# Performance work log

Hardware: AMD Instinct MI355X
Metric: run time of the kernel (lower is better)

The kernel has to match this reference:

```python
import jax, jax.numpy as jnp
import numpy as np
from jax import lax

B, L, D, E, K, H = 8, 1024, 256, 8, 2, 1024  # batch, seq(in_channel), in_dim, experts, top_k, out_channel/hidden
LMAX = L // 2  # largest expert input dim (factor i+2 = 2)
LENS = [L // (i + 2) for i in range(E)]


def setup_inputs() -> dict:
    key = jax.random.key(0)
    ks = jax.random.split(key, 12)
    x = jax.random.normal(ks[0], (B, L, D), dtype=jnp.float32)
    conv_ws = jax.random.normal(ks[1], (3, D, D, 3), dtype=jnp.float32) / np.sqrt(3 * D)
    conv_bs = jax.random.normal(ks[2], (3, D), dtype=jnp.float32) * 0.01
    fl_w = jax.random.normal(ks[3], (E, L), dtype=jnp.float32) / np.sqrt(L)
    fl_b = jax.random.normal(ks[4], (E,), dtype=jnp.float32) * 0.01
    # expert first-layer weights, zero-padded on input axis to LMAX (expert i uses L//(i+2) inputs)
    w1 = jax.random.normal(ks[5], (E, H, LMAX), dtype=jnp.float32) / np.sqrt(LMAX)
    col_mask = (np.arange(LMAX)[None, :] < np.array(LENS)[:, None]).astype(np.float32)  # [E, LMAX]
    w1 = w1 * jnp.asarray(col_mask)[:, None, :]
    b1 = jax.random.normal(ks[6], (E, H), dtype=jnp.float32) * 0.01
    w2 = jax.random.normal(ks[7], (E, H, H), dtype=jnp.float32) / np.sqrt(H)
    b2 = jax.random.normal(ks[8], (E, H), dtype=jnp.float32) * 0.01
    w3 = jax.random.normal(ks[9], (E, H, H), dtype=jnp.float32) / np.sqrt(H)
    b3 = jax.random.normal(ks[10], (E, H), dtype=jnp.float32) * 0.01
    return {"x": x, "conv_ws": conv_ws, "conv_bs": conv_bs, "fl_w": fl_w, "fl_b": fl_b,
            "w1": w1, "b1": b1, "w2": w2, "b2": b2, "w3": w3, "b3": b3}


def _gelu(v):
    return jax.nn.gelu(v, approximate=False)  # torch nn.GELU default is exact erf


def _forward(x, conv_ws, conv_bs, fl_w, fl_b, w1, b1, w2, b2, w3, b3):
    xt = jnp.transpose(x, (0, 2, 1))  # [B, D, L]
    # --- Router: 3 dilated causal-padded ('same') convs + GELU ---
    h = xt
    for i in range(3):
        d = 2 ** i
        h = lax.conv_general_dilated(h, conv_ws[i], window_strides=(1,), padding=[(d, d)],
                                     rhs_dilation=(d,), dimension_numbers=("NCH", "OIH", "NCH"))
        h = _gelu(h + conv_bs[i][None, :, None])
    logits = jax.nn.sigmoid(jnp.einsum("bdl,el->bde", h, fl_w) + fl_b)  # [B, D, E]
    prob = jax.nn.softmax(logits, axis=-1)
    top_val, top_idx = lax.top_k(prob, K)  # [B, D, K]
    top_val = top_val / jnp.sum(top_val, axis=-1, keepdims=True)
    # combine gate per expert: gates[b,d,e] = sum_k top_val * 1[top_idx==e]
    gates = jnp.sum(top_val[..., None] * jax.nn.one_hot(top_idx, E, dtype=top_val.dtype), axis=2)  # [B, D, E]
    # --- Per-expert downsample (avg_pool1d, kernel=stride=i+2), zero-padded to LMAX ---
    xs = []
    for i in range(E):
        f = i + 2
        Li = LENS[i]
        xd = xt[:, :, :Li * f].reshape(B, D, Li, f).mean(-1)  # [B, D, Li]
        xs.append(jnp.pad(xd, ((0, 0), (0, 0), (0, LMAX - Li))))
    xe = jnp.stack(xs)  # [E, B, D, LMAX]; pad cols align with zeroed w1 cols
    # --- Expert MLPs (dense compute, masked by gates; zero gate == token not routed) ---
    h1 = _gelu(jnp.einsum("ebdl,ehl->ebdh", xe, w1) + b1[:, None, None, :])
    h2 = _gelu(jnp.einsum("ebdh,egh->ebdg", h1, w2) + b2[:, None, None, :])
    h3 = jnp.einsum("ebdg,eog->ebdo", h2, w3) + b3[:, None, None, :]  # [E, B, D, H]
    out = jnp.einsum("ebdo,bde->bdo", h3, gates)  # scatter-add combine, [B, D, H]
    return jnp.transpose(out, (0, 2, 1))  # [B, L(out_channel), D]


def reference(x, conv_ws, conv_bs, fl_w, fl_b, w1, b1, w2, b2, w3, b3):
    return _forward(x, conv_ws, conv_bs, fl_w, fl_b, w1, b1, w2, b2, w3, b3)
```

## Files before the change

kernel.cpp:

```cpp
#include <hip/hip_runtime.h>
#include <math.h>

#define Bb 8
#define Ll 1024
#define Dd 256
#define Ee 8
#define Hh 1024
#define LMAXc 512
#define NTOK (Bb*Dd)
#define LPAD 1032
#define MAXTILES 72

typedef short bf16x8 __attribute__((ext_vector_type(8)));
typedef float f32x4 __attribute__((ext_vector_type(4)));
typedef unsigned short u16x8 __attribute__((ext_vector_type(8)));

__device__ __forceinline__ float gelu_f(float x) {
    return 0.5f * x * (1.0f + erff(x * 0.70710678118654752440f));
}
__device__ __forceinline__ unsigned short f2b(float x) {
    unsigned int u = __float_as_uint(x);
    return (unsigned short)((u + 0x7fffu + ((u >> 16) & 1u)) >> 16);
}
__device__ __forceinline__ float b2f(unsigned short h) {
    return __uint_as_float(((unsigned int)h) << 16);
}
__device__ __forceinline__ void gl_lds16(const void* g, void* l) {
    __builtin_amdgcn_global_load_lds((const __attribute__((address_space(1))) unsigned int*)g,
                                     (__attribute__((address_space(3))) unsigned int*)l, 16, 0, 0);
}
__device__ __forceinline__ void split_store(float4 v,
                                            unsigned short* __restrict__ hi,
                                            unsigned short* __restrict__ lo, int idx) {
    ushort2 h01, h23, l01, l23;
    unsigned short h;
    h = f2b(v.x); h01.x = h; l01.x = f2b(v.x - b2f(h));
    h = f2b(v.y); h01.y = h; l01.y = f2b(v.y - b2f(h));
    h = f2b(v.z); h23.x = h; l23.x = f2b(v.z - b2f(h));
    h = f2b(v.w); h23.y = h; l23.y = f2b(v.w - b2f(h));
    ((ushort2*)hi)[idx * 2] = h01; ((ushort2*)hi)[idx * 2 + 1] = h23;
    ((ushort2*)lo)[idx * 2] = l01; ((ushort2*)lo)[idx * 2 + 1] = l23;
}
__device__ __forceinline__ void cvt_store(float4 v, unsigned short* __restrict__ dst, int idx) {
    ushort2 h01, h23;
    h01.x = f2b(v.x); h01.y = f2b(v.y);
    h23.x = f2b(v.z); h23.y = f2b(v.w);
    ((ushort2*)dst)[idx * 2] = h01; ((ushort2*)dst)[idx * 2 + 1] = h23;
}

__global__ __launch_bounds__(256) void prep_all(
    const float* __restrict__ x, const float* __restrict__ cw,
    const float* __restrict__ w1, const float* __restrict__ w2,
    const float* __restrict__ w3,
    unsigned short* __restrict__ xhi, unsigned short* __restrict__ xlo,
    unsigned short* __restrict__ chi, unsigned short* __restrict__ clo,
    unsigned short* __restrict__ wchi, unsigned short* __restrict__ wclo,
    unsigned short* __restrict__ w1hi, unsigned short* __restrict__ w1lo,
    unsigned short* __restrict__ w2b, unsigned short* __restrict__ w3b,
    unsigned short* __restrict__ xe)
{
    int blk = blockIdx.x;
    int t = threadIdx.x;
    if (blk < 4096) {
        int u = blk;
        int e = u >> 9;
        int b = (u >> 6) & 7;
        int c = u & 63;
        int f = e + 2;
        int Li = Ll / f;
        int j0 = c * 8;
        if (j0 >= Li) return;
        int d = t;
        float invf = 1.0f / (float)f;
        int lim = Li - 1;
        float v[8] = {};
        for (int r = 0; r < f; ++r) {
            #pragma unroll
            for (int jj = 0; jj < 8; ++jj) {
                int j = j0 + jj; if (j > lim) j = lim;
                v[jj] += x[((size_t)(b * Ll + j * f + r)) * Dd + d];
            }
        }
        size_t obase = ((size_t)(e * NTOK + b * 256 + d)) * LMAXc + j0;
        if (j0 + 8 <= Li) {
            u16x8 hv;
            #pragma unroll
            for (int q = 0; q < 8; ++q) hv[q] = (short)f2b(v[q] * invf);
            *(u16x8*)(xe + obase) = hv;
        } else {
            for (int jj = 0; jj < Li - j0; ++jj)
                xe[obase + jj] = f2b(v[jj] * invf);
        }
    } else if (blk < 4128) {
        int u = (blk - 4096) * 256 + t;
        int f = u >> 11;
        int rem = u & 2047;
        int b = rem >> 8;
        int r2 = rem & 255;
        int row = r2 >> 5;
        int col = (r2 & 31) * 8;
        int padrow = (row < 4) ? row : (1024 + row);
        unsigned short* buf = (f == 0) ? xhi : (f == 1) ? xlo : (f == 2) ? chi : clo;
        u16x8 z = {0, 0, 0, 0, 0, 0, 0, 0};
        *(u16x8*)(buf + (size_t)(b * LPAD + padrow) * Dd + col) = z;
    } else if (blk < 4640) {
        int base = (blk - 4128) * 1024 + t;
        float4 v[4];
        #pragma unroll
        for (int it = 0; it < 4; ++it) v[it] = ((const float4*)x)[base + it * 256];
        #pragma unroll
        for (int it = 0; it < 4; ++it) {
            int idx = base + it * 256;
            int d4 = idx & 63;
            int l  = (idx >> 6) & 1023;
            int b  = idx >> 16;
            size_t o = ((size_t)(b * LPAD + 4 + l) * Dd + d4 * 4) >> 1;
            ushort2 h01, h23, l01, l23;
            unsigned short h;
            h = f2b(v[it].x); h01.x = h; l01.x = f2b(v[it].x - b2f(h));
            h = f2b(v[it].y); h01.y = h; l01.y = f2b(v[it].y - b2f(h));
            h = f2b(v[it].z); h23.x = h; l23.x = f2b(v[it].z - b2f(h));
            h = f2b(v[it].w); h23.y = h; l23.y = f2b(v[it].w - b2f(h));
            ((ushort2*)xhi)[o] = h01; ((ushort2*)xhi)[o + 1] = h23;
            ((ushort2*)xlo)[o] = l01; ((ushort2*)xlo)[o + 1] = l23;
        }
    } else if (blk < 5216) {
        int base = (blk - 4640) * 1024 + t;
        float vv[4];
        #pragma unroll
        for (int it = 0; it < 4; ++it) {
            int idx = base + it * 256;
            int i = idx & (Dd - 1);
            int o = (idx >> 8) & (Dd - 1);
            int lk = idx >> 16;
            int layer = lk / 3;
            int k = lk % 3;
            vv[it] = cw[(((size_t)layer * Dd + o) * Dd + i) * 3 + k];
        }
        #pragma unroll
        for (int it = 0; it < 4; ++it) {
            int idx = base + it * 256;
            unsigned short h = f2b(vv[it]);
            wchi[idx] = h;
            wclo[idx] = f2b(vv[it] - b2f(h));
        }
    } else if (blk < 6240) {
        int base = (blk - 5216) * 1024 + t;
        float4 v[4];
        #pragma unroll
        for (int it = 0; it < 4; ++it) v[it] = ((const float4*)w1)[base + it * 256];
        #pragma unroll
        for (int it = 0; it < 4; ++it) split_store(v[it], w1hi, w1lo, base + it * 256);
    } else if (blk < 8288) {
        int base = (blk - 6240) * 1024 + t;
        float4 v[4];
        #pragma unroll
        for (int it = 0; it < 4; ++it) v[it] = ((const float4*)w2)[base + it * 256];
        #pragma unroll
        for (int it = 0; it < 4; ++it) cvt_store(v[it], w2b, base + it * 256);
    } else {
        int base = (blk - 8288) * 1024 + t;
        float4 v[4];
        #pragma unroll
        for (int it = 0; it < 4; ++it) v[it] = ((const float4*)w3)[base + it * 256];
        #pragma unroll
        for (int it = 0; it < 4; ++it) cvt_store(v[it], w3b, base + it * 256);
    }
}

template<int MODE>
__global__ __launch_bounds__(256, 2) void conv_mfma(
    const unsigned short* __restrict__ inhi, const unsigned short* __restrict__ inlo,
    const unsigned short* __restrict__ whiL, const unsigned short* __restrict__ wloL,
    const float* __restrict__ bias,
    unsigned short* __restrict__ outhi, unsigned short* __restrict__ outlo,
    const float* __restrict__ flw, float* __restrict__ logits, int dil)
{
    __shared__ char smem[32768];
    char* sAhi = smem;
    char* sAlo = smem + 8192;
    char* sBhi = smem + 16384;
    char* sBlo = smem + 24576;

    const int t = threadIdx.x;
    const int lane = t & 63, w = t >> 6;
    const int r16 = lane & 15, quad = lane >> 4;
    const int wr = w >> 1, wc = w & 1;
    const int row0 = blockIdx.x * 64;
    const int col0 = blockIdx.y * 64;
    const int b = row0 >> 10, l0 = row0 & 1023;

    int aoff[2], boff[2];
    #pragma unroll
    for (int i = 0; i < 2; ++i) {
        int ra = wr * 32 + i * 16 + r16;
        aoff[i] = ra * 64 + ((quad ^ ((ra >> 1) & 3)) << 4);
        int rb = wc * 32 + i * 16 + r16;
        boff[i] = rb * 64 + ((quad ^ ((rb >> 1) & 3)) << 4);
    }
    const int rs = t >> 2, ce = ((t & 3) ^ ((rs >> 1) & 3)) << 3;
    const unsigned short* gAhi = inhi + (size_t)(b * LPAD + 4 + l0 + rs) * Dd + ce;
    const unsigned short* gAlo = inlo + (size_t)(b * LPAD + 4 + l0 + rs) * Dd + ce;

    f32x4 acc[2][2];
    const f32x4 zero4 = {0.f, 0.f, 0.f, 0.f};
    #pragma unroll
    for (int i = 0; i < 2; ++i)
        #pragma unroll
        for (int j = 0; j < 2; ++j) acc[i][j] = zero4;

    for (int tap = 0; tap < 3; ++tap) {
        const int sh = (tap - 1) * dil;
        const unsigned short* pAhi = gAhi + sh * Dd;
        const unsigned short* pAlo = gAlo + sh * Dd;
        const unsigned short* gBhi = whiL + ((size_t)tap * Dd + col0 + rs) * Dd + ce;
        const unsigned short* gBlo = wloL + ((size_t)tap * Dd + col0 + rs) * Dd + ce;
        for (int kb = 0; kb < Dd; kb += 64) {
            gl_lds16(pAhi + kb,      sAhi + (w << 10));
            gl_lds16(pAhi + kb + 32, sAhi + 4096 + (w << 10));
            gl_lds16(pAlo + kb,      sAlo + (w << 10));
            gl_lds16(pAlo + kb + 32, sAlo + 4096 + (w << 10));
            gl_lds16(gBhi + kb,      sBhi + (w << 10));
            gl_lds16(gBhi + kb + 32, sBhi + 4096 + (w << 10));
            gl_lds16(gBlo + kb,      sBlo + (w << 10));
            gl_lds16(gBlo + kb + 32, sBlo + 4096 + (w << 10));
            __syncthreads();
            #pragma unroll
            for (int h = 0; h < 2; ++h) {
                const int ho = h * 4096;
                bf16x8 ah[2], al[2], bh[2], bl[2];
                #pragma unroll
                for (int i = 0; i < 2; ++i) {
                    ah[i] = *(const bf16x8*)(sAhi + ho + aoff[i]);
                    al[i] = *(const bf16x8*)(sAlo + ho + aoff[i]);
                    bh[i] = *(const bf16x8*)(sBhi + ho + boff[i]);
                    bl[i] = *(const bf16x8*)(sBlo + ho + boff[i]);
                }
                #pragma unroll
                for (int mi = 0; mi < 2; ++mi)
                    #pragma unroll
                    for (int ni = 0; ni < 2; ++ni) {
                        acc[mi][ni] = __builtin_amdgcn_mfma_f32_16x16x32_bf16(ah[mi], bh[ni], acc[mi][ni], 0, 0, 0);
                        acc[mi][ni] = __builtin_amdgcn_mfma_f32_16x16x32_bf16(ah[mi], bl[ni], acc[mi][ni], 0, 0, 0);
                        acc[mi][ni] = __builtin_amdgcn_mfma_f32_16x16x32_bf16(al[mi], bh[ni], acc[mi][ni], 0, 0, 0);
                    }
            }
            __syncthreads();
        }
    }

    int cc[2]; float bv[2];
    #pragma unroll
    for (int ni = 0; ni < 2; ++ni) {
        cc[ni] = col0 + wc * 32 + ni * 16 + r16;
        bv[ni] = bias[cc[ni]];
    }
    if (MODE == 0) {
        #pragma unroll
        for (int mi = 0; mi < 2; ++mi) {
            int lb = l0 + wr * 32 + mi * 16 + quad * 4;
            #pragma unroll
            for (int reg = 0; reg < 4; ++reg) {
                int l = lb + reg;
                #pragma unroll
                for (int ni = 0; ni < 2; ++ni) {
                    float v = gelu_f(acc[mi][ni][reg] + bv[ni]);
                    size_t o = (size_t)(b * LPAD + 4 + l) * Dd + cc[ni];
                    unsigned short h = f2b(v);
                    outhi[o] = h;
                    outlo[o] = f2b(v - b2f(h));
                }
            }
        }
    } else {
        float* wl   = (float*)smem;
        float* slog = (float*)(smem + 2048);
        for (int i = t; i < 512; i += 256) {
            int ll = i >> 3, e = i & 7;
            wl[i] = flw[e * Ll + l0 + ll];
            slog[i] = 0.0f;
        }
        __syncthreads();
        float part[2][8];
        #pragma unroll
        for (int ni = 0; ni < 2; ++ni)
            #pragma unroll
            for (int e = 0; e < 8; ++e) part[ni][e] = 0.0f;
        #pragma unroll
        for (int mi = 0; mi < 2; ++mi) {
            #pragma unroll
            for (int reg = 0; reg < 4; ++reg) {
                int ll = wr * 32 + mi * 16 + quad * 4 + reg;
                #pragma unroll
                for (int ni = 0; ni < 2; ++ni) {
                    float v = gelu_f(acc[mi][ni][reg] + bv[ni]);
                    #pragma unroll
                    for (int e = 0; e < 8; ++e) part[ni][e] += v * wl[ll * 8 + e];
                }
            }
        }
        #pragma unroll
        for (int ni = 0; ni < 2; ++ni) {
            int dl = wc * 32 + ni * 16 + r16;
            #pragma unroll
            for (int e = 0; e < 8; ++e) atomicAdd(&slog[dl * 8 + e], part[ni][e]);
        }
        __syncthreads();
        for (int i = t; i < 512; i += 256) {
            int dl = i >> 3, e = i & 7;
            atomicAdd(&logits[(size_t)(b * Dd + col0 + dl) * Ee + e], slog[i]);
        }
    }
}

template<int MODE, int GATHER, int TWOPASS>
__global__ __launch_bounds__(256, 4) void gemm_sp(
    const unsigned short* __restrict__ AG,
    const unsigned short* __restrict__ BhiG, const unsigned short* __restrict__ BloG,
    const float* __restrict__ biasG, const float* __restrict__ gates,
    const int* __restrict__ cntG, const int* __restrict__ listG,
    const int* __restrict__ tileTab, const int* __restrict__ ntiles,
    unsigned short* __restrict__ Cout, float* __restrict__ outf,
    int M, int N, int K)
{
    if (blockIdx.y >= ntiles[0]) return;
    const int desc = tileTab[blockIdx.y];
    const int e = desc >> 16;
    const int row0 = (desc & 0xffff) * 64;
    const int cn = cntG[e];

    constexpr int NCH = TWOPASS ? 2 : 4;
    __shared__ char smem[TWOPASS ? 24576 : 32768];
    char* sA   = smem;
    char* sBhi = smem + NCH * 4096;
    char* sBlo = smem + 2 * NCH * 4096;

    const unsigned short* Bhi = BhiG + (size_t)e * N * K;
    const unsigned short* Blo = TWOPASS ? (BloG + (size_t)e * N * K) : nullptr;
    const float* bias = biasG + (size_t)e * N;

    int Keff = K;
    if (GATHER) {
        int Li = Ll / (e + 2);
        Keff = ((Li + 63) >> 6) << 6;
    }

    const int t = threadIdx.x;
    const int lane = t & 63, w = t >> 6;
    const int r16 = lane & 15, quad = lane >> 4;
    const int wr = w >> 1, wc = w & 1;
    const int col0 = blockIdx.x * 64;

    int aoff[2], boff[2];
    #pragma unroll
    for (int i = 0; i < 2; ++i) {
        int ra = wr * 32 + i * 16 + r16;
        aoff[i] = ra * 64 + ((quad ^ ((ra >> 1) & 3)) << 4);
        int rb = wc * 32 + i * 16 + r16;
        boff[i] = rb * 64 + ((quad ^ ((rb >> 1) & 3)) << 4);
    }
    const int r0s = t >> 2, c0s = ((t & 3) ^ ((r0s >> 1) & 3)) << 3;
    int ri = row0 + r0s; if (ri > cn - 1) ri = cn - 1;
    const int ar = GATHER ? listG[e * NTOK + ri] : ri;
    const unsigned short* gA  = AG + ((size_t)e * M + ar) * K + c0s;
    const unsigned short* gB  = Bhi + (size_t)(col0 + r0s) * K + c0s;
    const unsigned short* gBl = TWOPASS ? (Blo + (size_t)(col0 + r0s) * K + c0s) : nullptr;
    const int wofs = w << 10;

    f32x4 acc[2][2];
    const f32x4 zero4 = {0.f, 0.f, 0.f, 0.f};
    #pragma unroll
    for (int i = 0; i < 2; ++i)
        #pragma unroll
        for (int j = 0; j < 2; ++j) acc[i][j] = zero4;

    for (int k0 = 0; k0 < Keff; k0 += NCH * 32) {
        #pragma unroll
        for (int c = 0; c < NCH; ++c) {
            gl_lds16(gA + k0 + c * 32, sA + c * 4096 + wofs);
            gl_lds16(gB + k0 + c * 32, sBhi + c * 4096 + wofs);
        }
        if (TWOPASS) {
            #pragma unroll
            for (int c = 0; c < NCH; ++c)
                gl_lds16(gBl + k0 + c * 32, sBlo + c * 4096 + wofs);
        }
        __syncthreads();
        #pragma unroll
        for (int h = 0; h < NCH; ++h) {
            const int ho = h * 4096;
            bf16x8 ah[2], bh[2];
            #pragma unroll
            for (int i = 0; i < 2; ++i) {
                ah[i] = *(const bf16x8*)(sA + ho + aoff[i]);
                bh[i] = *(const bf16x8*)(sBhi + ho + boff[i]);
            }
            #pragma unroll
            for (int mi = 0; mi < 2; ++mi)
                #pragma unroll
                for (int ni = 0; ni < 2; ++ni)
                    acc[mi][ni] = __builtin_amdgcn_mfma_f32_16x16x32_bf16(ah[mi], bh[ni], acc[mi][ni], 0, 0, 0);
            if (TWOPASS) {
                bf16x8 bl[2];
                #pragma unroll
                for (int i = 0; i < 2; ++i) bl[i] = *(const bf16x8*)(sBlo + ho + boff[i]);
                #pragma unroll
                for (int mi = 0; mi < 2; ++mi)
                    #pragma unroll
                    for (int ni = 0; ni < 2; ++ni)
                        acc[mi][ni] = __builtin_amdgcn_mfma_f32_16x16x32_bf16(ah[mi], bl[ni], acc[mi][ni], 0, 0, 0);
            }
        }
        __syncthreads();
    }

    int cc[2]; float bv[2];
    #pragma unroll
    for (int ni = 0; ni < 2; ++ni) {
        cc[ni] = col0 + wc * 32 + ni * 16 + r16;
        bv[ni] = bias[cc[ni]];
    }
    if (MODE == 0) {
        unsigned short* CE = Cout + (size_t)e * M * N;
        #pragma unroll
        for (int mi = 0; mi < 2; ++mi) {
            int rb = row0 + wr * 32 + mi * 16 + quad * 4;
            #pragma unroll
            for (int reg = 0; reg < 4; ++reg) {
                size_t roff = (size_t)(rb + reg) * N;
                #pragma unroll
                for (int ni = 0; ni < 2; ++ni)
                    CE[roff + cc[ni]] = f2b(gelu_f(acc[mi][ni][reg] + bv[ni]));
            }
        }
    } else {
        #pragma unroll
        for (int mi = 0; mi < 2; ++mi) {
            int rb = row0 + wr * 32 + mi * 16 + quad * 4;
            #pragma unroll
            for (int reg = 0; reg < 4; ++reg) {
                int i = rb + reg;
                if (i < cn) {
                    int tok = listG[e * NTOK + i];
                    float g = gates[(size_t)tok * Ee + e];
                    size_t roff = (size_t)tok * N;
                    #pragma unroll
                    for (int ni = 0; ni < 2; ++ni)
                        atomicAdd(&outf[roff + cc[ni]], g * (acc[mi][ni][reg] + bv[ni]));
                }
            }
        }
    }
}


__global__ __launch_bounds__(1024) void gates_final(const float* __restrict__ logits,
                                                    const float* __restrict__ fl_b,
                                                    float* __restrict__ gates,
                                                    int* __restrict__ cnt,
                                                    int* __restrict__ list,
                                                    int* __restrict__ tileTab,
                                                    int* __restrict__ ntiles) {
    __shared__ int scnt[Ee];
    if (threadIdx.x < Ee) scnt[threadIdx.x] = 0;
    __syncthreads();
    const int lane = threadIdx.x & 63;
    const unsigned long long ltmask = (1ull << lane) - 1ull;

    for (int tok = threadIdx.x; tok < NTOK; tok += 1024) {
        float s[Ee];
        #pragma unroll
        for (int e = 0; e < Ee; ++e) {
            float z = logits[tok * Ee + e] + fl_b[e];
            s[e] = 1.0f / (1.0f + expf(-z));
        }
        float mx = s[0];
        #pragma unroll
        for (int e = 1; e < Ee; ++e) mx = fmaxf(mx, s[e]);
        float p[Ee];
        #pragma unroll
        for (int e = 0; e < Ee; ++e) p[e] = expf(s[e] - mx);
        int i1 = 0;
        #pragma unroll
        for (int e = 1; e < Ee; ++e) if (p[e] > p[i1]) i1 = e;
        int i2 = (i1 == 0) ? 1 : 0;
        #pragma unroll
        for (int e = 0; e < Ee; ++e) {
            if (e == i1 || e == i2) continue;
            if (p[e] > p[i2]) i2 = e;
        }
        float inv = 1.0f / (p[i1] + p[i2]);
        #pragma unroll
        for (int e = 0; e < Ee; ++e) gates[tok * Ee + e] = 0.0f;
        gates[tok * Ee + i1] = p[i1] * inv;
        gates[tok * Ee + i2] = p[i2] * inv;

        #pragma unroll
        for (int slot = 0; slot < 2; ++slot) {
            int ie = slot ? i2 : i1;
            for (int e = 0; e < Ee; ++e) {
                unsigned long long m = __ballot(ie == e);
                if (m) {
                    int leader = __ffsll((long long)m) - 1;
                    int base = 0;
                    if (lane == leader) base = atomicAdd(&scnt[e], (int)__popcll(m));
                    base = __shfl(base, leader);
                    if (ie == e) {
                        int pos = base + (int)__popcll(m & ltmask);
                        list[e * NTOK + pos] = tok;
                    }
                }
            }
        }
    }
    __syncthreads();
    if (threadIdx.x < Ee) cnt[threadIdx.x] = scnt[threadIdx.x];
    if (threadIdx.x == 0) {
        int nt = 0;
        for (int e = 0; e < Ee; ++e) {
            int c = scnt[e];
            for (int m = 0; m * 64 < c; ++m) tileTab[nt++] = (e << 16) | m;
        }
        ntiles[0] = nt;
    }
}

__global__ __launch_bounds__(256) void transpose_out(const float* __restrict__ outacc,
                                                     float* __restrict__ out) {
    __shared__ float tile[32][33];
    int b = blockIdx.z;
    int d0 = blockIdx.x * 32;
    int o0 = blockIdx.y * 32;
    int tx = threadIdx.x & 31, ty = threadIdx.x >> 5;
    for (int i = 0; i < 32; i += 8)
        tile[ty + i][tx] = outacc[((size_t)b * Dd + d0 + ty + i) * Hh + o0 + tx];
    __syncthreads();
    for (int i = 0; i < 32; i += 8)
        out[((size_t)b * Hh + o0 + ty + i) * Dd + d0 + tx] = tile[tx][ty + i];
}

extern "C" void kernel_launch(void* const* d_in, const int* in_sizes, int n_in,
                              void* d_out, int out_size, void* d_ws, size_t ws_size,
                              hipStream_t stream) {
    const float* x       = (const float*)d_in[0];
    const float* conv_w  = (const float*)d_in[1];
    const float* conv_b  = (const float*)d_in[2];
    const float* fl_w    = (const float*)d_in[3];
    const float* fl_b    = (const float*)d_in[4];
    const float* w1      = (const float*)d_in[5];
    const float* b1      = (const float*)d_in[6];
    const float* w2      = (const float*)d_in[7];
    const float* b2      = (const float*)d_in[8];
    const float* w3      = (const float*)d_in[9];
    const float* b3      = (const float*)d_in[10];
    float* out = (float*)d_out;

    char* ws = (char*)d_ws;
    unsigned short* xphi = (unsigned short*)(ws);
    unsigned short* xplo = (unsigned short*)(ws + 4227072);
    unsigned short* cphi = (unsigned short*)(ws + 8454144);
    unsigned short* cplo = (unsigned short*)(ws + 12681216);
    unsigned short* wchi = (unsigned short*)(ws + 16908288);
    unsigned short* wclo = (unsigned short*)(ws + 18087936);
    unsigned short* h1   = (unsigned short*)(ws);
    unsigned short* h2   = (unsigned short*)(ws + 33554432);
    unsigned short* xe   = (unsigned short*)(ws + 67108864);
    unsigned short* w1hi = (unsigned short*)(ws + 83886080);
    unsigned short* w1lo = (unsigned short*)(ws + 92274688);
    unsigned short* w2b  = (unsigned short*)(ws + 100663296);
    unsigned short* w3b  = (unsigned short*)(ws + 117440512);
    float* logits  = (float*)(ws + 134217728);
    int*   cnt     = (int*)(ws + 134283264);
    int*   ntiles  = (int*)(ws + 134283296);
    int*   tileTab = (int*)(ws + 134283328);
    float* gates   = (float*)(ws + 134284288);
    int*   list    = (int*)(ws + 134349824);
    float* outacc  = (float*)(ws);

    hipMemsetAsync(logits, 0, 65536 + 64, stream);

    prep_all<<<10336, 256, 0, stream>>>(x, conv_w, w1, w2, w3,
                                        xphi, xplo, cphi, cplo, wchi, wclo,
                                        w1hi, w1lo, w2b, w3b, xe);

    const int WL = 3 * Dd * Dd;
    conv_mfma<0><<<dim3(Bb * Ll / 64, Dd / 64), 256, 0, stream>>>(
        xphi, xplo, wchi + 0 * WL, wclo + 0 * WL, conv_b + 0 * Dd, cphi, cplo, nullptr, nullptr, 1);
    conv_mfma<0><<<dim3(Bb * Ll / 64, Dd / 64), 256, 0, stream>>>(
        cphi, cplo, wchi + 1 * WL, wclo + 1 * WL, conv_b + 1 * Dd, xphi, xplo, nullptr, nullptr, 2);
    conv_mfma<1><<<dim3(Bb * Ll / 64, Dd / 64), 256, 0, stream>>>(
        xphi, xplo, wchi + 2 * WL, wclo + 2 * WL, conv_b + 2 * Dd, nullptr, nullptr, fl_w, logits, 4);

    gates_final<<<1, 1024, 0, stream>>>(logits, fl_b, gates, cnt, list, tileTab, ntiles);

    gemm_sp<0, 1, 1><<<dim3(16, MAXTILES), 256, 0, stream>>>(
        xe, w1hi, w1lo, b1, nullptr, cnt, list, tileTab, ntiles, h1, nullptr, NTOK, Hh, LMAXc);

    gemm_sp<0, 0, 0><<<dim3(16, MAXTILES), 256, 0, stream>>>(
        h1, w2b, nullptr, b2, nullptr, cnt, list, tileTab, ntiles, h2, nullptr, NTOK, Hh, Hh);

    hipMemsetAsync(outacc, 0, (size_t)NTOK * Hh * sizeof(float), stream);

    gemm_sp<1, 0, 0><<<dim3(16, MAXTILES), 256, 0, stream>>>(
        h2, w3b, nullptr, b3, gates, cnt, list, tileTab, ntiles, nullptr, outacc, NTOK, Hh, Hh);

    transpose_out<<<dim3(Dd / 32, Hh / 32, Bb), 256, 0, stream>>>(outacc, out);
}
```

Measured before the change: 308.2 us.

## Overlap expert weight bf16 conversion with conv kernels via extra grid blocks

Moves the w1/w2/w3 fp32-to-bf16 conversion out of the prep kernel and into extra blockIdx.y rows of the three conv kernels, so the memory-bound conversion runs alongside the compute-bound conv MFMA blocks. It also widens the x and conv-weight split conversions to 8-element vector stores. The conv kernels gain a template flag and more blocks, which may perturb scheduling, but the prep launch shrinks.

New measurement: 309.5 us. No clear change (+0.4%).

```diff
diff --git a/kernel.cpp b/kernel.cpp
--- a/kernel.cpp
+++ b/kernel.cpp
@@ -29,34 +29,12 @@
     __builtin_amdgcn_global_load_lds((const __attribute__((address_space(1))) unsigned int*)g,
                                      (__attribute__((address_space(3))) unsigned int*)l, 16, 0, 0);
 }
-__device__ __forceinline__ void split_store(float4 v,
-                                            unsigned short* __restrict__ hi,
-                                            unsigned short* __restrict__ lo, int idx) {
-    ushort2 h01, h23, l01, l23;
-    unsigned short h;
-    h = f2b(v.x); h01.x = h; l01.x = f2b(v.x - b2f(h));
-    h = f2b(v.y); h01.y = h; l01.y = f2b(v.y - b2f(h));
-    h = f2b(v.z); h23.x = h; l23.x = f2b(v.z - b2f(h));
-    h = f2b(v.w); h23.y = h; l23.y = f2b(v.w - b2f(h));
-    ((ushort2*)hi)[idx * 2] = h01; ((ushort2*)hi)[idx * 2 + 1] = h23;
-    ((ushort2*)lo)[idx * 2] = l01; ((ushort2*)lo)[idx * 2 + 1] = l23;
-}
-__device__ __forceinline__ void cvt_store(float4 v, unsigned short* __restrict__ dst, int idx) {
-    ushort2 h01, h23;
-    h01.x = f2b(v.x); h01.y = f2b(v.y);
-    h23.x = f2b(v.z); h23.y = f2b(v.w);
-    ((ushort2*)dst)[idx * 2] = h01; ((ushort2*)dst)[idx * 2 + 1] = h23;
-}
 
 __global__ __launch_bounds__(256) void prep_all(
     const float* __restrict__ x, const float* __restrict__ cw,
-    const float* __restrict__ w1, const float* __restrict__ w2,
-    const float* __restrict__ w3,
     unsigned short* __restrict__ xhi, unsigned short* __restrict__ xlo,
     unsigned short* __restrict__ chi, unsigned short* __restrict__ clo,
     unsigned short* __restrict__ wchi, unsigned short* __restrict__ wclo,
-    unsigned short* __restrict__ w1hi, unsigned short* __restrict__ w1lo,
-    unsigned short* __restrict__ w2b, unsigned short* __restrict__ w3b,
     unsigned short* __restrict__ xe)
 {
     int blk = blockIdx.x;
@@ -103,80 +81,100 @@
         unsigned short* buf = (f == 0) ? xhi : (f == 1) ? xlo : (f == 2) ? chi : clo;
         u16x8 z = {0, 0, 0, 0, 0, 0, 0, 0};
         *(u16x8*)(buf + (size_t)(b * LPAD + padrow) * Dd + col) = z;
-    } else if (blk < 4640) {
-        int base = (blk - 4128) * 1024 + t;
-        float4 v[4];
-        #pragma unroll
-        for (int it = 0; it < 4; ++it) v[it] = ((const float4*)x)[base + it * 256];
+    } else if (blk < 4384) {
+        int cb = blk - 4128;
+        const float4* s4 = (const float4*)x;
+        size_t ob = (size_t)cb * 1024 + t;
+        float4 v[8];
         #pragma unroll
         for (int it = 0; it < 4; ++it) {
-            int idx = base + it * 256;
-            int d4 = idx & 63;
-            int l  = (idx >> 6) & 1023;
-            int b  = idx >> 16;
-            size_t o = ((size_t)(b * LPAD + 4 + l) * Dd + d4 * 4) >> 1;
-            ushort2 h01, h23, l01, l23;
-            unsigned short h;
-            h = f2b(v[it].x); h01.x = h; l01.x = f2b(v[it].x - b2f(h));
-            h = f2b(v[it].y); h01.y = h; l01.y = f2b(v[it].y - b2f(h));
-            h = f2b(v[it].z); h23.x = h; l23.x = f2b(v[it].z - b2f(h));
-            h = f2b(v[it].w); h23.y = h; l23.y = f2b(v[it].w - b2f(h));
-            ((ushort2*)xhi)[o] = h01; ((ushort2*)xhi)[o + 1] = h23;
-            ((ushort2*)xlo)[o] = l01; ((ushort2*)xlo)[o + 1] = l23;
-        }
-    } else if (blk < 5216) {
-        int base = (blk - 4640) * 1024 + t;
-        float vv[4];
+            v[2 * it]     = s4[(ob + it * 256) * 2];
+            v[2 * it + 1] = s4[(ob + it * 256) * 2 + 1];
+        }
         #pragma unroll
         for (int it = 0; it < 4; ++it) {
-            int idx = base + it * 256;
+            size_t o = ob + it * 256;
+            int d8 = (int)(o & 31), l = (int)((o >> 5) & 1023), b = (int)(o >> 15);
+            size_t ooff = (size_t)(b * LPAD + 4 + l) * Dd + d8 * 8;
+            float vv[8] = {v[2*it].x, v[2*it].y, v[2*it].z, v[2*it].w,
+                           v[2*it+1].x, v[2*it+1].y, v[2*it+1].z, v[2*it+1].w};
+            u16x8 hv, lv;
+            #pragma unroll
+            for (int q = 0; q < 8; ++q) {
+                unsigned short h = f2b(vv[q]);
+                hv[q] = (short)h;
+                lv[q] = (short)f2b(vv[q] - b2f(h));
+            }
+            *(u16x8*)(xhi + ooff) = hv;
+            *(u16x8*)(xlo + ooff) = lv;
+        }
+    } else {
+        int cb = blk - 4384;
+        int idx0 = (cb * 256 + t) * 8;
+        float vv[8];
+        #pragma unroll
+        for (int q = 0; q < 8; ++q) {
+            int idx = idx0 + q;
             int i = idx & (Dd - 1);
             int o = (idx >> 8) & (Dd - 1);
             int lk = idx >> 16;
             int layer = lk / 3;
             int k = lk % 3;
-            vv[it] = cw[(((size_t)layer * Dd + o) * Dd + i) * 3 + k];
-        }
-        #pragma unroll
-        for (int it = 0; it < 4; ++it) {
-            int idx = base + it * 256;
-            unsigned short h = f2b(vv[it]);
-            wchi[idx] = h;
-            wclo[idx] = f2b(vv[it] - b2f(h));
-        }
-    } else if (blk < 6240) {
-        int base = (blk - 5216) * 1024 + t;
-        float4 v[4];
-        #pragma unroll
-        for (int it = 0; it < 4; ++it) v[it] = ((const float4*)w1)[base + it * 256];
-        #pragma unroll
-        for (int it = 0; it < 4; ++it) split_store(v[it], w1hi, w1lo, base + it * 256);
-    } else if (blk < 8288) {
-        int base = (blk - 6240) * 1024 + t;
-        float4 v[4];
-        #pragma unroll
-        for (int it = 0; it < 4; ++it) v[it] = ((const float4*)w2)[base + it * 256];
-        #pragma unroll
-        for (int it = 0; it < 4; ++it) cvt_store(v[it], w2b, base + it * 256);
-    } else {
-        int base = (blk - 8288) * 1024 + t;
-        float4 v[4];
-        #pragma unroll
-        for (int it = 0; it < 4; ++it) v[it] = ((const float4*)w3)[base + it * 256];
-        #pragma unroll
-        for (int it = 0; it < 4; ++it) cvt_store(v[it], w3b, base + it * 256);
-    }
-}
-
-template<int MODE>
+            vv[q] = cw[(((size_t)layer * Dd + o) * Dd + i) * 3 + k];
+        }
+        u16x8 hv, lv;
+        #pragma unroll
+        for (int q = 0; q < 8; ++q) {
+            unsigned short h = f2b(vv[q]);
+            hv[q] = (short)h;
+            lv[q] = (short)f2b(vv[q] - b2f(h));
+        }
+        *(u16x8*)(wchi + idx0) = hv;
+        *(u16x8*)(wclo + idx0) = lv;
+    }
+}
+
+template<int MODE, int CVT>
 __global__ __launch_bounds__(256, 2) void conv_mfma(
     const unsigned short* __restrict__ inhi, const unsigned short* __restrict__ inlo,
     const unsigned short* __restrict__ whiL, const unsigned short* __restrict__ wloL,
     const float* __restrict__ bias,
     unsigned short* __restrict__ outhi, unsigned short* __restrict__ outlo,
-    const float* __restrict__ flw, float* __restrict__ logits, int dil)
+    const float* __restrict__ flw, float* __restrict__ logits,
+    const float* __restrict__ cvsrc, unsigned short* __restrict__ cvd1,
+    unsigned short* __restrict__ cvd2, int dil)
 {
     __shared__ char smem[32768];
+
+    if (CVT && blockIdx.y >= (Dd / 64)) {
+        int cb = (blockIdx.y - Dd / 64) * 128 + blockIdx.x;
+        int t = threadIdx.x;
+        const float4* s4 = (const float4*)cvsrc;
+        size_t ob = (size_t)cb * 1024 + t;
+        float4 v[8];
+        #pragma unroll
+        for (int it = 0; it < 4; ++it) {
+            v[2 * it]     = s4[(ob + it * 256) * 2];
+            v[2 * it + 1] = s4[(ob + it * 256) * 2 + 1];
+        }
+        #pragma unroll
+        for (int it = 0; it < 4; ++it) {
+            size_t o = ob + it * 256;
+            float vv[8] = {v[2*it].x, v[2*it].y, v[2*it].z, v[2*it].w,
+                           v[2*it+1].x, v[2*it+1].y, v[2*it+1].z, v[2*it+1].w};
+            u16x8 hv, lv;
+            #pragma unroll
+            for (int q = 0; q < 8; ++q) {
+                unsigned short h = f2b(vv[q]);
+                hv[q] = (short)h;
+                if (CVT == 1) lv[q] = (short)f2b(vv[q] - b2f(h));
+            }
+            *(u16x8*)(cvd1 + o * 8) = hv;
+            if (CVT == 1) *(u16x8*)(cvd2 + o * 8) = lv;
+        }
+        return;
+    }
+
     char* sAhi = smem;
     char* sAlo = smem + 8192;
     char* sBhi = smem + 16384;
@@ -579,17 +577,19 @@
 
     hipMemsetAsync(logits, 0, 65536 + 64, stream);
 
-    prep_all<<<10336, 256, 0, stream>>>(x, conv_w, w1, w2, w3,
-                                        xphi, xplo, cphi, cplo, wchi, wclo,
-                                        w1hi, w1lo, w2b, w3b, xe);
+    prep_all<<<4672, 256, 0, stream>>>(x, conv_w, xphi, xplo, cphi, cplo,
+                                       wchi, wclo, xe);
 
     const int WL = 3 * Dd * Dd;
-    conv_mfma<0><<<dim3(Bb * Ll / 64, Dd / 64), 256, 0, stream>>>(
-        xphi, xplo, wchi + 0 * WL, wclo + 0 * WL, conv_b + 0 * Dd, cphi, cplo, nullptr, nullptr, 1);
-    conv_mfma<0><<<dim3(Bb * Ll / 64, Dd / 64), 256, 0, stream>>>(
-        cphi, cplo, wchi + 1 * WL, wclo + 1 * WL, conv_b + 1 * Dd, xphi, xplo, nullptr, nullptr, 2);
-    conv_mfma<1><<<dim3(Bb * Ll / 64, Dd / 64), 256, 0, stream>>>(
-        xphi, xplo, wchi + 2 * WL, wclo + 2 * WL, conv_b + 2 * Dd, nullptr, nullptr, fl_w, logits, 4);
+    conv_mfma<0, 1><<<dim3(Bb * Ll / 64, Dd / 64 + 4), 256, 0, stream>>>(
+        xphi, xplo, wchi + 0 * WL, wclo + 0 * WL, conv_b + 0 * Dd, cphi, cplo,
+        nullptr, nullptr, w1, w1hi, w1lo, 1);
+    conv_mfma<0, 2><<<dim3(Bb * Ll / 64, Dd / 64 + 8), 256, 0, stream>>>(
+        cphi, cplo, wchi + 1 * WL, wclo + 1 * WL, conv_b + 1 * Dd, xphi, xplo,
+        nullptr, nullptr, w2, w2b, nullptr, 2);
+    conv_mfma<1, 2><<<dim3(Bb * Ll / 64, Dd / 64 + 8), 256, 0, stream>>>(
+        xphi, xplo, wchi + 2 * WL, wclo + 2 * WL, conv_b + 2 * Dd, nullptr, nullptr,
+        fl_w, logits, w3, w3b, nullptr, 4);
 
     gates_final<<<1, 1024, 0, stream>>>(logits, fl_b, gates, cnt, list, tileTab, ntiles);
 
```
